# Kernel optimization log

Hardware: AMD Instinct MI355X
Metric: run time of the kernel (lower is better)

Reference implementation:

```python
import jax, jax.numpy as jnp
import numpy as np

B, T, D, H = 2, 2048, 768, 12
d = D // H
FRAG, K_SEL, G = 16, 6, 4
TOP_U, PROTO = 12, 32
ALPHA, GAMMA = 0.2, 0.2
W_MEAN, W_MAX, W_TOPK, W_STD = 1.0, 0.6, 0.4, 0.2
TOPK_FRAC = 0.2
TAU = 8.0
NEG = -1e9


def _norm(x, eps=1e-6):
    return x / jnp.maximum(jnp.linalg.norm(x, axis=-1, keepdims=True), eps)


def setup_inputs():
    key = jax.random.key(0)
    ks = jax.random.split(key, 5)
    s = 0.02
    return {
        'x': jax.random.normal(ks[0], (B, T, D), jnp.float32),
        'Wq': jax.random.normal(ks[1], (D, D), jnp.float32) * s,
        'bq': jnp.zeros((D,), jnp.float32),
        'Wk': jax.random.normal(ks[2], (D, D), jnp.float32) * s,
        'bk': jnp.zeros((D,), jnp.float32),
        'Wv': jax.random.normal(ks[3], (D, D), jnp.float32) * s,
        'bv': jnp.zeros((D,), jnp.float32),
        'Wo': jax.random.normal(ks[4], (D, D), jnp.float32) * s,
        'bo': jnp.zeros((D,), jnp.float32),
    }


def _forward(x, Wq, bq, Wk, bk, Wv, bv, Wo, bo):
    scaling = d ** -0.5

    def shape(t):  # [B,T,D] -> [B*H,T,d]  (BartAttention._shape layout: (b,h))
        return t.reshape(B, T, H, d).transpose(0, 2, 1, 3).reshape(B * H, T, d)

    q = shape((x @ Wq.T + bq) * scaling)
    k = shape(x @ Wk.T + bk)
    v = shape(x @ Wv.T + bv)

    # ---- windowed local candidate indices (build_indices_encoder) ----
    half = FRAG // 2
    t_ar = jnp.arange(T)
    starts = jnp.clip(t_ar - half, 0, T - FRAG)
    idx = starts[:, None] + jnp.arange(FRAG)[None, :]            # [T,F]
    prior = jnp.exp(-jnp.abs(idx - t_ar[:, None]).astype(jnp.float32) / TAU)

    keys_win = k[:, idx]                                          # [BH,T,F,d]
    scores_win = jnp.einsum('btd,btfd->btf', q, keys_win)
    blended = scores_win + ALPHA * prior[None]

    # ---- greedy diversity-penalized top-k (WindowSelector.select_greedy) ----
    kvn = _norm(keys_win)
    f_ar = jnp.arange(FRAG)
    tmp = blended
    sels = []
    for r in range(K_SEL):
        j = jnp.argmax(tmp, -1)                                   # [BH,T]
        sels.append(j)
        if r < K_SEL - 1:
            sel_vec = jnp.take_along_axis(kvn, j[:, :, None, None], axis=2)[:, :, 0]
            cos = jnp.maximum(jnp.sum(kvn * sel_vec[:, :, None, :], -1), 0.0)
            tmp = tmp - GAMMA * cos
        tmp = jnp.where(f_ar[None, None, :] == j[..., None], NEG, tmp)
    sel_local = jnp.stack(sels, -1)                               # [BH,T,k]
    sel_abs = jnp.take_along_axis(
        jnp.broadcast_to(idx[None], (B * H, T, FRAG)), sel_local, axis=-1)

    # ---- per-head global tokens (GlobalChooser.choose_packed) ----
    # faithful to torch: key_states.view(H, bsz, Tk, d).mean(dim=1)
    Kmean = k.reshape(H, B, T, d).mean(1)
    Kbar = _norm(Kmean)
    q_summary = _norm(q.reshape(H, B, T, d).mean(1))
    idxp = jnp.round(jnp.linspace(0.0, T - 1, PROTO)).astype(jnp.int32)
    Qp = q_summary[:, idxp]                                       # [H,P,d]
    S = jax.nn.relu(jnp.einsum('hkd,hpd->hkp', Kbar, Qp))         # [H,T,P]
    kq = max(1, int(round(PROTO * TOPK_FRAC)))
    u = (W_MEAN * S.mean(-1) + W_MAX * S.max(-1)
         + W_TOPK * jax.lax.top_k(S, kq)[0].mean(-1)
         + W_STD * jnp.std(S, axis=-1, ddof=1))
    U = min(TOP_U, T)
    u_vals, top_idx = jax.lax.top_k(u, U)                         # [H,U]
    S_sub = jnp.take_along_axis(S, top_idx[:, :, None], axis=1)   # [H,U,P]
    hr = jnp.arange(H)
    m = jnp.zeros((H, PROTO), S.dtype)
    blocked = jnp.zeros((H, U), bool)
    chosen = []
    for r in range(G):  # greedy facility-location
        gains = jnp.maximum(S_sub - m[:, None, :], 0.0).sum(-1)
        gains = jnp.where(blocked, NEG, gains)
        j = jnp.argmax(gains, 1)
        chosen.append(j)
        blocked = blocked.at[hr, j].set(True)
        m = jnp.maximum(m, S_sub[hr, j])
    chosen_abs = jnp.take_along_axis(top_idx, jnp.stack(chosen, 1), axis=1)  # [H,G]

    # ---- sparse attention over local + global candidates ----
    glob = jnp.broadcast_to(chosen_abs[None], (B, H, G)).reshape(B * H, G)
    cand = jnp.concatenate(
        [sel_abs, jnp.broadcast_to(glob[:, None, :], (B * H, T, G))], -1)  # [BH,T,k+g]
    Ksel = jax.vmap(lambda kk, ii: kk[ii])(k, cand)               # [BH,T,k+g,d]
    Vsel = jax.vmap(lambda vv, ii: vv[ii])(v, cand)
    attn = jax.nn.softmax(jnp.einsum('btd,btcd->btc', q, Ksel), axis=-1)
    out = jnp.einsum('btc,btcd->btd', attn, Vsel)
    out = out.reshape(B, H, T, d).transpose(0, 2, 1, 3).reshape(B, T, D)
    return out @ Wo.T + bo


def reference(x, Wq, bq, Wk, bk, Wv, bv, Wo, bo):
    return _forward(x, Wq, bq, Wk, bk, Wv, bv, Wo, bo)
```

## Files before the change

### kernel.cpp

```cpp
#include <hip/hip_runtime.h>
#include <math.h>

#define TSEQ 2048
#define DM   768
#define NH   12
#define HD   64
#define NBH  24
#define WN   589824

typedef __attribute__((ext_vector_type(8))) short short8;
typedef __attribute__((ext_vector_type(8))) _Float16 half8;
typedef __attribute__((ext_vector_type(4))) float f32x4;

#define MFMA_F16(a, b, c)  __builtin_amdgcn_mfma_f32_16x16x32_f16(a, b, c, 0, 0, 0)

__constant__ int c_idxp[32] = {0,66,132,198,264,330,396,462,528,594,660,726,
  792,858,924,990,1057,1123,1189,1255,1321,1387,1453,1519,1585,1651,1717,1783,
  1849,1915,1981,2047};

template <int CTRL>
__device__ __forceinline__ float dppf(float x) {
  return __int_as_float(__builtin_amdgcn_mov_dpp(__float_as_int(x), CTRL, 0xF, 0xF, true));
}
template <int CTRL>
__device__ __forceinline__ int dppi(int x) {
  return __builtin_amdgcn_mov_dpp(x, CTRL, 0xF, 0xF, true);
}
__device__ __forceinline__ float wsum(float v) {
  v += dppf<0x121>(v);
  v += dppf<0x122>(v);
  v += dppf<0x124>(v);
  v += dppf<0x128>(v);
  v += __shfl_xor(v, 16, 64);
  v += __shfl_xor(v, 32, 64);
  return v;
}
__device__ __forceinline__ float wmaxr(float v) {
  v = fmaxf(v, dppf<0x121>(v));
  v = fmaxf(v, dppf<0x122>(v));
  v = fmaxf(v, dppf<0x124>(v));
  v = fmaxf(v, dppf<0x128>(v));
  v = fmaxf(v, __shfl_xor(v, 16, 64));
  v = fmaxf(v, __shfl_xor(v, 32, 64));
  return v;
}
__device__ __forceinline__ float rowsum16(float v) {
  v += dppf<0x121>(v); v += dppf<0x122>(v);
  v += dppf<0x124>(v); v += dppf<0x128>(v);
  return v;
}
__device__ __forceinline__ float rowmax16(float v) {
  v = fmaxf(v, dppf<0x121>(v)); v = fmaxf(v, dppf<0x122>(v));
  v = fmaxf(v, dppf<0x124>(v)); v = fmaxf(v, dppf<0x128>(v));
  return v;
}
__device__ __forceinline__ int rowmin16i(int v) {
  v = min(v, dppi<0x121>(v)); v = min(v, dppi<0x122>(v));
  v = min(v, dppi<0x124>(v)); v = min(v, dppi<0x128>(v));
  return v;
}

__device__ __forceinline__ void split16(const float4& v0, const float4& v1,
                                        ushort* ph, ushort* pl) {
  float xs[8] = {v0.x, v0.y, v0.z, v0.w, v1.x, v1.y, v1.z, v1.w};
  half8 h, l;
#pragma unroll
  for (int j = 0; j < 8; ++j) {
    _Float16 hb = (_Float16)xs[j];
    h[j] = hb;
    float d = xs[j] - (float)hb;
    l[j] = (_Float16)d;
  }
  *(half8*)ph = h;
  *(half8*)pl = l;
}

__device__ __forceinline__ int lds_idx(int row, int chunk ) {
  int line = row >> 1;
  int c8 = ((row & 1) << 2) | chunk;
  return line * 64 + ((c8 ^ (line & 7)) << 3);
}
__device__ __forceinline__ int qoff(int p, int c8) {
  return p * 64 + (((c8 ^ (p & 7)) & 7) << 3);
}

__global__ __launch_bounds__(256) void convert_kernel(
    const float* __restrict__ x,
    const float* __restrict__ W0, const float* __restrict__ W1,
    const float* __restrict__ W2, const float* __restrict__ W3,
    ushort* __restrict__ Xh, ushort* __restrict__ Xl,
    ushort* __restrict__ wsp) {
  int z = blockIdx.y;
  size_t base = (size_t)(blockIdx.x * 256 + threadIdx.x) * 8;
  if (z == 0) {
    float4 v0 = *(const float4*)(x + base);
    float4 v1 = *(const float4*)(x + base + 4);
    split16(v0, v1, Xh + base, Xl + base);
  } else {
    if (base >= WN) return;
    int mi = z - 1;
    const float* s = (mi == 0) ? W0 : (mi == 1) ? W1 : (mi == 2) ? W2 : W3;
    ushort* h = wsp + (size_t)mi * 2 * WN;
    float4 v0 = *(const float4*)(s + base);
    float4 v1 = *(const float4*)(s + base + 4);
    split16(v0, v1, h + base, h + WN + base);
  }
}

template <int MODE, int NPROD>
__device__ __forceinline__ void gemm_mfma_body(
    const ushort* __restrict__ Agh, const ushort* __restrict__ Agl,
    const ushort* __restrict__ Bgh, const ushort* __restrict__ Bgl,
    const float* __restrict__ bias, float* __restrict__ dst, float scale,
    int mblk, int nblk, ushort* lds) {
  const int tid = threadIdx.x;
  const int lane = tid & 63;
  const int w = tid >> 6;
  const int wr = w >> 1, wc = w & 1;
  const int lrow = lane & 15, kq = lane >> 4;
  constexpr int ABUF = 4096;
  constexpr int BBUF = 2048;
  ushort* Ahs = lds;
  ushort* Als = Ahs + ABUF;
  ushort* Bhs = lds + 2 * ABUF;
  ushort* Bls = Bhs + BBUF;

  const int arow = tid >> 2;
  const int achk = tid & 3;
  const int aoff0 = lds_idx(arow, achk);
  const int aoff1 = lds_idx(arow + 64, achk);
  const int boff = lds_idx(arow, achk);

  const size_t a0 = (size_t)(mblk + arow) * DM + achk * 8;
  const size_t a1 = (size_t)(mblk + 64 + arow) * DM + achk * 8;
  const size_t b0 = (size_t)(nblk + arow) * DM + achk * 8;

  f32x4 acc[4][2];
#pragma unroll
  for (int i = 0; i < 4; ++i)
#pragma unroll
    for (int j = 0; j < 2; ++j) {
      f32x4 z = {0.f, 0.f, 0.f, 0.f};
      acc[i][j] = z;
    }

  short8 pah0 = *(const short8*)(Agh + a0), pah1 = *(const short8*)(Agh + a1);
  short8 pal0 = *(const short8*)(Agl + a0), pal1 = *(const short8*)(Agl + a1);
  short8 pbh = *(const short8*)(Bgh + b0);
  short8 pbl = *(const short8*)(Bgl + b0);

  for (int k0 = 0; k0 < DM; k0 += 32) {
    __syncthreads();
    *(short8*)&Ahs[aoff0] = pah0; *(short8*)&Ahs[aoff1] = pah1;
    *(short8*)&Als[aoff0] = pal0; *(short8*)&Als[aoff1] = pal1;
    *(short8*)&Bhs[boff] = pbh;
    *(short8*)&Bls[boff] = pbl;
    __syncthreads();
    if (k0 + 32 < DM) {
      pah0 = *(const short8*)(Agh + a0 + k0 + 32);
      pah1 = *(const short8*)(Agh + a1 + k0 + 32);
      pal0 = *(const short8*)(Agl + a0 + k0 + 32);
      pal1 = *(const short8*)(Agl + a1 + k0 + 32);
      pbh = *(const short8*)(Bgh + b0 + k0 + 32);
      pbl = *(const short8*)(Bgl + b0 + k0 + 32);
    }
    half8 afh[4], afl[4];
#pragma unroll
    for (int fi = 0; fi < 4; ++fi) {
      int o = lds_idx(wr * 64 + fi * 16 + lrow, kq);
      afh[fi] = *(const half8*)&Ahs[o];
      afl[fi] = *(const half8*)&Als[o];
    }
#pragma unroll
    for (int fj = 0; fj < 2; ++fj) {
      int o = lds_idx(wc * 32 + fj * 16 + lrow, kq);
      half8 bfh = *(const half8*)&Bhs[o];
      half8 bfl = *(const half8*)&Bls[o];
#pragma unroll
      for (int fi = 0; fi < 4; ++fi) {
        acc[fi][fj] = MFMA_F16(afh[fi], bfh, acc[fi][fj]);
        acc[fi][fj] = MFMA_F16(afl[fi], bfh, acc[fi][fj]);
        acc[fi][fj] = MFMA_F16(afh[fi], bfl, acc[fi][fj]);
        if (NPROD == 4) {
          acc[fi][fj] = MFMA_F16(afl[fi], bfl, acc[fi][fj]);
        }
      }
    }
  }

#pragma unroll
  for (int fj = 0; fj < 2; ++fj) {
    int col = nblk + wc * 32 + fj * 16 + lrow;
    float bv = bias[col];
#pragma unroll
    for (int fi = 0; fi < 4; ++fi) {
#pragma unroll
      for (int reg = 0; reg < 4; ++reg) {
        int row = mblk + wr * 64 + fi * 16 + kq * 4 + reg;
        float o = (acc[fi][fj][reg] + bv) * scale;
        if (MODE == 0) {
          dst[(size_t)row * DM + col] = o;
        } else {
          int b_ = row >> 11, t = row & (TSEQ - 1);
          int h = col >> 6, dd = col & 63;
          dst[(((size_t)(b_ * NH + h)) * TSEQ + t) * HD + dd] = o;
        }
      }
    }
  }
}

__global__ __launch_bounds__(256) void qkv_kernel(
    const ushort* __restrict__ Xh, const ushort* __restrict__ Xl,
    const ushort* __restrict__ wsp,
    const float* __restrict__ bq, float* __restrict__ qd,
    const float* __restrict__ bk, float* __restrict__ kd,
    const float* __restrict__ bv, float* __restrict__ vd) {
  __shared__ ushort lds[2 * 4096 + 2 * 2048];
  int lid = blockIdx.x + 12 * blockIdx.y + 384 * blockIdx.z;
  int swz = (lid & 7) * 144 + (lid >> 3);
  int z = swz / 384;
  int rem = swz - z * 384;
  int wy = rem / 12, wx = rem - wy * 12;
  const ushort* Bb = wsp + (size_t)z * 2 * WN;
  if (z == 2) {
    gemm_mfma_body<1, 3>(Xh, Xl, Bb, Bb + WN,
                         bv, vd, 1.0f, wy * 128, wx * 64, lds);
  } else {
    gemm_mfma_body<1, 4>(Xh, Xl, Bb, Bb + WN,
                         z ? bk : bq, z ? kd : qd, z ? 1.0f : 0.125f,
                         wy * 128, wx * 64, lds);
  }
}

__global__ __launch_bounds__(256) void oproj_kernel(
    const ushort* __restrict__ Ph, const ushort* __restrict__ Pl,
    const ushort* __restrict__ wsp,
    const float* __restrict__ bias, float* __restrict__ dst) {
  __shared__ ushort lds[2 * 4096 + 2 * 2048];
  int lid = blockIdx.x + 12 * blockIdx.y;
  int swz = (lid & 7) * 48 + (lid >> 3);
  int wy = swz / 12, wx = swz - wy * 12;
  const ushort* Bb = wsp + (size_t)3 * 2 * WN;
  gemm_mfma_body<0, 3>(Ph, Pl, Bb, Bb + WN,
                       bias, dst, 1.0f, wy * 128, wx * 64, lds);
}

__global__ __launch_bounds__(256) void window_kernel(
    const float* __restrict__ q, const float* __restrict__ k,
    int* __restrict__ sel) {
  int wid = blockIdx.x * 4 + (threadIdx.x >> 6);
  int lane = threadIdx.x & 63;
  int f = lane & 15, kq = lane >> 4;
  int bh = wid >> 11, t = wid & (TSEQ - 1);
  int start = t - 8;
  if (start < 0) start = 0;
  if (start > TSEQ - 16) start = TSEQ - 16;

  const float* kp = k + ((size_t)bh * TSEQ + start + f) * HD + kq * 8;
  const float* qp = q + ((size_t)bh * TSEQ + t) * HD + kq * 8;
  float kv[16], qv[16];
  *(float4*)&kv[0]  = *(const float4*)(kp + 0);
  *(float4*)&kv[4]  = *(const float4*)(kp + 4);
  *(float4*)&kv[8]  = *(const float4*)(kp + 32);
  *(float4*)&kv[12] = *(const float4*)(kp + 36);
  *(float4*)&qv[0]  = *(const float4*)(qp + 0);
  *(float4*)&qv[4]  = *(const float4*)(qp + 4);
  *(float4*)&qv[8]  = *(const float4*)(qp + 32);
  *(float4*)&qv[12] = *(const float4*)(qp + 36);

  float sp = 0.f, np = 0.f;
#pragma unroll
  for (int i = 0; i < 16; ++i) { sp = fmaf(qv[i], kv[i], sp); np = fmaf(kv[i], kv[i], np); }
  sp += __shfl_xor(sp, 16, 64); sp += __shfl_xor(sp, 32, 64);
  np += __shfl_xor(np, 16, 64); np += __shfl_xor(np, 32, 64);
  float nrm = fmaxf(sqrtf(np), 1e-6f);
  float kn[16];
#pragma unroll
  for (int i = 0; i < 16; ++i) kn[i] = kv[i] / nrm;

  half8 h0, l0, h1, l1;
#pragma unroll
  for (int j = 0; j < 8; ++j) {
    _Float16 hb = (_Float16)kn[j];
    h0[j] = hb;
    l0[j] = (_Float16)(kn[j] - (float)hb);
    _Float16 hb1 = (_Float16)kn[8 + j];
    h1[j] = hb1;
    l1[j] = (_Float16)(kn[8 + j] - (float)hb1);
  }
  f32x4 g = {0.f, 0.f, 0.f, 0.f};
  g = MFMA_F16(h0, h0, g); g = MFMA_F16(h1, h1, g);
  g = MFMA_F16(l0, h0, g); g = MFMA_F16(l1, h1, g);
  g = MFMA_F16(h0, l0, g); g = MFMA_F16(h1, l1, g);
  g = MFMA_F16(l0, l0, g); g = MFMA_F16(l1, l1, g);

  int dist = start + f - t; if (dist < 0) dist = -dist;
  float tmp = sp + 0.2f * expf(-(float)dist * 0.125f);

  int* selp = sel + ((size_t)bh * TSEQ + t) * 6;
#pragma unroll
  for (int r = 0; r < 6; ++r) {
    float best = tmp; int bj = f;
    {
      float ov = dppf<0x121>(best); int oi = dppi<0x121>(bj);
      if (ov > best || (ov == best && oi < bj)) { best = ov; bj = oi; }
      ov = dppf<0x122>(best); oi = dppi<0x122>(bj);
      if (ov > best || (ov == best && oi < bj)) { best = ov; bj = oi; }
      ov = dppf<0x124>(best); oi = dppi<0x124>(bj);
      if (ov > best || (ov == best && oi < bj)) { best = ov; bj = oi; }
      ov = dppf<0x128>(best); oi = dppi<0x128>(bj);
      if (ov > best || (ov == best && oi < bj)) { best = ov; bj = oi; }
    }
    if (lane == 0) selp[r] = start + bj;
    if (r < 5) {
      float s01 = (bj & 1) ? g[1] : g[0];
      float s23 = (bj & 1) ? g[3] : g[2];
      float gsel = (bj & 2) ? s23 : s01;
      float grow = __shfl(gsel, ((bj >> 2) << 4) | f, 64);
      tmp -= 0.2f * fmaxf(grow, 0.f);
    }
    if (f == bj) tmp = -1e9f;
  }
}

__global__ __launch_bounds__(256) void qp_kernel(const float* __restrict__ q,
                                                 ushort* __restrict__ Qph,
                                                 ushort* __restrict__ Qpl) {
  int wid = blockIdx.x * 4 + (threadIdx.x >> 6);
  int lane = threadIdx.x & 63;
  int a = wid >> 5, p = wid & 31;
  int t = c_idxp[p];
  float v = 0.5f * (q[((size_t)(2 * a) * TSEQ + t) * HD + lane] +
                    q[((size_t)(2 * a + 1) * TSEQ + t) * HD + lane]);
  float n2 = wsum(v * v);
  float nrm = fmaxf(sqrtf(n2), 1e-6f);
  float qn = v / nrm;
  _Float16 hb = (_Float16)qn;
  float d = qn - (float)hb;
  size_t idx = ((size_t)a * 32 + p) * HD + lane;
  Qph[idx] = __builtin_bit_cast(ushort, hb);
  _Float16 lb = (_Float16)d;
  Qpl[idx] = __builtin_bit_cast(ushort, lb);
}

__global__ __launch_bounds__(256) void proto_score_kernel(
    const float* __restrict__ k,
    const ushort* __restrict__ Qph, const ushort* __restrict__ Qpl,
    float* __restrict__ S, float* __restrict__ u) {
  int a = blockIdx.y;
  __shared__ ushort Qh[2048], Ql[2048];
  {
    int p = threadIdx.x >> 3, c8 = threadIdx.x & 7;
    size_t src = (size_t)a * 2048 + p * 64 + c8 * 8;
    *(short8*)&Qh[qoff(p, c8)] = *(const short8*)(Qph + src);
    *(short8*)&Ql[qoff(p, c8)] = *(const short8*)(Qpl + src);
  }
  __syncthreads();

  int wv = threadIdx.x >> 6, lane = threadIdx.x & 63;
  int f = lane & 15, kq = lane >> 4;
  int tbase = blockIdx.x * 64 + wv * 16;
  int tl = tbase + f;

  const float* k0p = k + ((size_t)(2 * a) * TSEQ + tl) * HD + kq * 8;
  const float* k1p = k + ((size_t)(2 * a + 1) * TSEQ + tl) * HD + kq * 8;
  float km[16];
  {
    float4 x0 = *(const float4*)(k0p + 0),  y0 = *(const float4*)(k1p + 0);
    float4 x1 = *(const float4*)(k0p + 4),  y1 = *(const float4*)(k1p + 4);
    float4 x2 = *(const float4*)(k0p + 32), y2 = *(const float4*)(k1p + 32);
    float4 x3 = *(const float4*)(k0p + 36), y3 = *(const float4*)(k1p + 36);
    km[0] = 0.5f*(x0.x+y0.x); km[1] = 0.5f*(x0.y+y0.y);
    km[2] = 0.5f*(x0.z+y0.z); km[3] = 0.5f*(x0.w+y0.w);
    km[4] = 0.5f*(x1.x+y1.x); km[5] = 0.5f*(x1.y+y1.y);
    km[6] = 0.5f*(x1.z+y1.z); km[7] = 0.5f*(x1.w+y1.w);
    km[8] = 0.5f*(x2.x+y2.x); km[9] = 0.5f*(x2.y+y2.y);
    km[10] = 0.5f*(x2.z+y2.z); km[11] = 0.5f*(x2.w+y2.w);
    km[12] = 0.5f*(x3.x+y3.x); km[13] = 0.5f*(x3.y+y3.y);
    km[14] = 0.5f*(x3.z+y3.z); km[15] = 0.5f*(x3.w+y3.w);
  }
  float np = 0.f;
#pragma unroll
  for (int i = 0; i < 16; ++i) np = fmaf(km[i], km[i], np);
  np += __shfl_xor(np, 16, 64); np += __shfl_xor(np, 32, 64);
  float nrm = fmaxf(sqrtf(np), 1e-6f);

  half8 ah[2], al[2];
#pragma unroll
  for (int s = 0; s < 2; ++s)
#pragma unroll
    for (int j = 0; j < 8; ++j) {
      float x = km[s * 8 + j] / nrm;
      _Float16 hb = (_Float16)x;
      ah[s][j] = hb;
      al[s][j] = (_Float16)(x - (float)hb);
    }

  f32x4 acc0 = {0.f, 0.f, 0.f, 0.f}, acc1 = {0.f, 0.f, 0.f, 0.f};
#pragma unroll
  for (int s = 0; s < 2; ++s) {
    half8 b0h = *(const half8*)&Qh[qoff(f, s * 4 + kq)];
    half8 b0l = *(const half8*)&Ql[qoff(f, s * 4 + kq)];
    half8 b1h = *(const half8*)&Qh[qoff(16 + f, s * 4 + kq)];
    half8 b1l = *(const half8*)&Ql[qoff(16 + f, s * 4 + kq)];
    acc0 = MFMA_F16(ah[s], b0h, acc0);
    acc0 = MFMA_F16(al[s], b0h, acc0);
    acc0 = MFMA_F16(ah[s], b0l, acc0);
    acc0 = MFMA_F16(al[s], b0l, acc0);
    acc1 = MFMA_F16(ah[s], b1h, acc1);
    acc1 = MFMA_F16(al[s], b1h, acc1);
    acc1 = MFMA_F16(ah[s], b1l, acc1);
    acc1 = MFMA_F16(al[s], b1l, acc1);
  }

#pragma unroll
  for (int reg = 0; reg < 4; ++reg) {
    float s0 = fmaxf(acc0[reg], 0.f);
    float s1 = fmaxf(acc1[reg], 0.f);
    int t = tbase + kq * 4 + reg;
    size_t srow = ((size_t)a * TSEQ + t) * 32;
    S[srow + f] = s0;
    S[srow + 16 + f] = s1;
    float mean = rowsum16(s0 + s1) / 32.0f;
    float mx = rowmax16(fmaxf(s0, s1));
    float cur0 = s0, cur1 = s1;
    float topsum = 0.f;
#pragma unroll
    for (int r = 0; r < 6; ++r) {
      float mm = rowmax16(fmaxf(cur0, cur1));
      topsum += mm;
      int i0 = rowmin16i((cur0 == mm) ? f : 999);
      int i1 = rowmin16i((cur1 == mm) ? f : 999);
      bool take0 = (i0 < 999);
      if (take0 && f == i0) cur0 = -1e30f;
      if (!take0 && f == i1) cur1 = -1e30f;
    }
    float d0 = s0 - mean, d1 = s1 - mean;
    float sd = sqrtf(rowsum16(d0 * d0 + d1 * d1) / 31.0f);
    float uval = ((1.0f * mean + 0.6f * mx) + 0.4f * (topsum / 6.0f)) + 0.2f * sd;
    if (f == 0) u[(size_t)a * TSEQ + t] = uval;
  }
}

__global__ void head_select_kernel(const float* __restrict__ u,
                                   const float* __restrict__ S,
                                   int* __restrict__ glob) {
  int a = blockIdx.x;
  int lane = threadIdx.x;
  float uv[32];
#pragma unroll
  for (int c = 0; c < 32; ++c) uv[c] = u[(size_t)a * TSEQ + c * 64 + lane];
  unsigned removed = 0;
  int tidx = 0;
#pragma unroll
  for (int r = 0; r < 12; ++r) {
    float best = -1e30f; int bidx = 1 << 30;
#pragma unroll
    for (int c = 0; c < 32; ++c) {
      if (!((removed >> c) & 1u)) {
        float vv = uv[c]; int gi = c * 64 + lane;
        if (vv > best || (vv == best && gi < bidx)) { best = vv; bidx = gi; }
      }
    }
#pragma unroll
    for (int mS = 1; mS < 64; mS <<= 1) {
      float ov = __shfl_xor(best, mS, 64);
      int oi = __shfl_xor(bidx, mS, 64);
      if (ov > best || (ov == best && oi < bidx)) { best = ov; bidx = oi; }
    }
    if (lane == (bidx & 63)) removed |= 1u << (bidx >> 6);
    if (lane == r) tidx = bidx;
  }
  float srow[12];
#pragma unroll
  for (int r = 0; r < 12; ++r) {
    int tr = __shfl(tidx, r, 64);
    srow[r] = (lane < 32) ? S[((size_t)a * TSEQ + tr) * 32 + lane] : 0.f;
  }
  float m = 0.f;
  unsigned blocked = 0;
#pragma unroll
  for (int g = 0; g < 4; ++g) {
    float gains[12];
#pragma unroll
    for (int r = 0; r < 12; ++r) {
      float gr = (lane < 32) ? fmaxf(srow[r] - m, 0.f) : 0.f;
      gains[r] = wsum(gr);
    }
    float best = -1e30f; int bj = 0;
#pragma unroll
    for (int r = 0; r < 12; ++r) {
      float vv = ((blocked >> r) & 1u) ? -1e9f : gains[r];
      if (vv > best) { best = vv; bj = r; }
    }
    blocked |= 1u << bj;
#pragma unroll
    for (int r = 0; r < 12; ++r) m = (r == bj) ? fmaxf(m, srow[r]) : m;
    int gidx = __shfl(tidx, bj, 64);
    if (lane == 0) glob[a * 4 + g] = gidx;
  }
}

__global__ __launch_bounds__(256) void attend_kernel(
    const float* __restrict__ q, const float* __restrict__ k,
    const float* __restrict__ v, const int* __restrict__ sel,
    const int* __restrict__ glob, ushort* __restrict__ Ph,
    ushort* __restrict__ Pl) {
  int wid = blockIdx.x * 4 + (threadIdx.x >> 6);
  int lane = threadIdx.x & 63;
  int bh = wid >> 11, t = wid & (TSEQ - 1);
  int h = bh % NH, b = bh / NH;
  float qv = q[((size_t)bh * TSEQ + t) * HD + lane];
  int cand[10];
  const int* selp = sel + ((size_t)bh * TSEQ + t) * 6;
#pragma unroll
  for (int c = 0; c < 6; ++c) cand[c] = selp[c];
#pragma unroll
  for (int c = 0; c < 4; ++c) cand[6 + c] = glob[h * 4 + c];
  float sc[10];
#pragma unroll
  for (int c = 0; c < 10; ++c) {
    float kv = k[((size_t)bh * TSEQ + cand[c]) * HD + lane];
    sc[c] = wsum(qv * kv);
  }
  float mx = sc[0];
#pragma unroll
  for (int c = 1; c < 10; ++c) mx = fmaxf(mx, sc[c]);
  float e[10], den = 0.f;
#pragma unroll
  for (int c = 0; c < 10; ++c) { e[c] = expf(sc[c] - mx); den += e[c]; }
  float o = 0.f;
#pragma unroll
  for (int c = 0; c < 10; ++c) {
    float w = e[c] / den;
    o += w * v[((size_t)bh * TSEQ + cand[c]) * HD + lane];
  }
  size_t idx = ((size_t)b * TSEQ + t) * DM + h * HD + lane;
  _Float16 hb = (_Float16)o;
  float d = o - (float)hb;
  Ph[idx] = __builtin_bit_cast(ushort, hb);
  _Float16 lb = (_Float16)d;
  Pl[idx] = __builtin_bit_cast(ushort, lb);
}

extern "C" void kernel_launch(void* const* d_in, const int* in_sizes, int n_in,
                              void* d_out, int out_size, void* d_ws, size_t ws_size,
                              hipStream_t stream) {
  const float* x  = (const float*)d_in[0];
  const float* Wq = (const float*)d_in[1];
  const float* bq = (const float*)d_in[2];
  const float* Wk = (const float*)d_in[3];
  const float* bk = (const float*)d_in[4];
  const float* Wv = (const float*)d_in[5];
  const float* bv = (const float*)d_in[6];
  const float* Wo = (const float*)d_in[7];
  const float* bo = (const float*)d_in[8];
  float* out = (float*)d_out;

  float* ws = (float*)d_ws;
  const size_t QKV = (size_t)NBH * TSEQ * HD;
  float* qb = ws;
  float* kb = qb + QKV;
  float* vb = kb + QKV;
  float* slotA = vb + QKV;
  float* QpSlot = slotA + QKV;
  float* S  = QpSlot + (size_t)NH * 32 * HD;
  float* u  = S + (size_t)NH * TSEQ * 32;
  int* sel  = (int*)(u + (size_t)NH * TSEQ);
  int* glob = sel + (size_t)NBH * TSEQ * 6;
  ushort* wsp = (ushort*)(glob + 64);

  ushort* Xh = (ushort*)slotA;
  ushort* Xl = Xh + QKV;
  ushort* Ph = Xh;
  ushort* Pl = Xl;
  ushort* Qph = (ushort*)QpSlot;
  ushort* Qpl = Qph + (size_t)NH * 32 * HD;

  convert_kernel<<<dim3(1536, 5), 256, 0, stream>>>(
      x, Wq, Wk, Wv, Wo, Xh, Xl, wsp);
  qkv_kernel<<<dim3(12, 32, 3), 256, 0, stream>>>(
      Xh, Xl, wsp, bq, qb, bk, kb, bv, vb);
  window_kernel<<<12288, 256, 0, stream>>>(qb, kb, sel);
  qp_kernel<<<96, 256, 0, stream>>>(qb, Qph, Qpl);
  proto_score_kernel<<<dim3(32, NH), 256, 0, stream>>>(kb, Qph, Qpl, S, u);
  head_select_kernel<<<NH, 64, 0, stream>>>(u, S, glob);
  attend_kernel<<<12288, 256, 0, stream>>>(qb, kb, vb, sel, glob, Ph, Pl);
  oproj_kernel<<<dim3(12, 32), 256, 0, stream>>>(Ph, Pl, wsp, bo, out);
}
```

Measured before the change: 217.1 us.

## Fuse window, prototype and head-select kernels into one launch with last-block election

Merges the window-selection, prototype-query normalisation, prototype scoring and head-select kernels into a single select_kernel. Block ranges are dispatched by blockIdx. Each prototype-scoring block recomputes the normalised prototype queries into LDS itself, and the last block per head (found with an atomic counter) runs the greedy head selection. The weight conversion grid is compacted so no blocks go idle. This removes three kernel launches and their gaps, at the cost of a memset, threadfence/atomic traffic, and redundant prototype-query computation in every scoring block.

```diff
diff --git a/kernel.cpp b/kernel.cpp
--- a/kernel.cpp
+++ b/kernel.cpp
@@ -35,15 +35,6 @@
   v += __shfl_xor(v, 32, 64);
   return v;
 }
-__device__ __forceinline__ float wmaxr(float v) {
-  v = fmaxf(v, dppf<0x121>(v));
-  v = fmaxf(v, dppf<0x122>(v));
-  v = fmaxf(v, dppf<0x124>(v));
-  v = fmaxf(v, dppf<0x128>(v));
-  v = fmaxf(v, __shfl_xor(v, 16, 64));
-  v = fmaxf(v, __shfl_xor(v, 32, 64));
-  return v;
-}
 __device__ __forceinline__ float rowsum16(float v) {
   v += dppf<0x121>(v); v += dppf<0x122>(v);
   v += dppf<0x124>(v); v += dppf<0x128>(v);
@@ -90,15 +81,16 @@
     const float* __restrict__ W2, const float* __restrict__ W3,
     ushort* __restrict__ Xh, ushort* __restrict__ Xl,
     ushort* __restrict__ wsp) {
-  int z = blockIdx.y;
-  size_t base = (size_t)(blockIdx.x * 256 + threadIdx.x) * 8;
-  if (z == 0) {
+  int bid = blockIdx.x;
+  if (bid < 1536) {
+    size_t base = ((size_t)bid * 256 + threadIdx.x) * 8;
     float4 v0 = *(const float4*)(x + base);
     float4 v1 = *(const float4*)(x + base + 4);
     split16(v0, v1, Xh + base, Xl + base);
   } else {
-    if (base >= WN) return;
-    int mi = z - 1;
+    int r = bid - 1536;
+    int mi = r / 288, sub = r - mi * 288;
+    size_t base = ((size_t)sub * 256 + threadIdx.x) * 8;
     const float* s = (mi == 0) ? W0 : (mi == 1) ? W1 : (mi == 2) ? W2 : W3;
     ushort* h = wsp + (size_t)mi * 2 * WN;
     float4 v0 = *(const float4*)(s + base);
@@ -246,121 +238,127 @@
                        bias, dst, 1.0f, wy * 128, wx * 64, lds);
 }
 
-__global__ __launch_bounds__(256) void window_kernel(
+__global__ __launch_bounds__(256) void select_kernel(
     const float* __restrict__ q, const float* __restrict__ k,
-    int* __restrict__ sel) {
-  int wid = blockIdx.x * 4 + (threadIdx.x >> 6);
-  int lane = threadIdx.x & 63;
+    int* __restrict__ sel, float* __restrict__ S, float* __restrict__ u,
+    int* __restrict__ glob, int* __restrict__ cnt) {
+  __shared__ ushort Qh[2048], Ql[2048];
+  int wv = threadIdx.x >> 6, lane = threadIdx.x & 63;
+
+  if (blockIdx.x < 12288) {
+    int wid = blockIdx.x * 4 + wv;
+    int f = lane & 15, kq = lane >> 4;
+    int bh = wid >> 11, t = wid & (TSEQ - 1);
+    int start = t - 8;
+    if (start < 0) start = 0;
+    if (start > TSEQ - 16) start = TSEQ - 16;
+
+    const float* kp = k + ((size_t)bh * TSEQ + start + f) * HD + kq * 8;
+    const float* qp = q + ((size_t)bh * TSEQ + t) * HD + kq * 8;
+    float kv[16], qv[16];
+    *(float4*)&kv[0]  = *(const float4*)(kp + 0);
+    *(float4*)&kv[4]  = *(const float4*)(kp + 4);
+    *(float4*)&kv[8]  = *(const float4*)(kp + 32);
+    *(float4*)&kv[12] = *(const float4*)(kp + 36);
+    *(float4*)&qv[0]  = *(const float4*)(qp + 0);
+    *(float4*)&qv[4]  = *(const float4*)(qp + 4);
+    *(float4*)&qv[8]  = *(const float4*)(qp + 32);
+    *(float4*)&qv[12] = *(const float4*)(qp + 36);
+
+    float sp = 0.f, np = 0.f;
+#pragma unroll
+    for (int i = 0; i < 16; ++i) { sp = fmaf(qv[i], kv[i], sp); np = fmaf(kv[i], kv[i], np); }
+    sp += __shfl_xor(sp, 16, 64); sp += __shfl_xor(sp, 32, 64);
+    np += __shfl_xor(np, 16, 64); np += __shfl_xor(np, 32, 64);
+    float nrm = fmaxf(sqrtf(np), 1e-6f);
+    float kn[16];
+#pragma unroll
+    for (int i = 0; i < 16; ++i) kn[i] = kv[i] / nrm;
+
+    half8 h0, l0, h1, l1;
+#pragma unroll
+    for (int j = 0; j < 8; ++j) {
+      _Float16 hb = (_Float16)kn[j];
+      h0[j] = hb;
+      l0[j] = (_Float16)(kn[j] - (float)hb);
+      _Float16 hb1 = (_Float16)kn[8 + j];
+      h1[j] = hb1;
+      l1[j] = (_Float16)(kn[8 + j] - (float)hb1);
+    }
+    f32x4 g = {0.f, 0.f, 0.f, 0.f};
+    g = MFMA_F16(h0, h0, g); g = MFMA_F16(h1, h1, g);
+    g = MFMA_F16(l0, h0, g); g = MFMA_F16(l1, h1, g);
+    g = MFMA_F16(h0, l0, g); g = MFMA_F16(h1, l1, g);
+    g = MFMA_F16(l0, l0, g); g = MFMA_F16(l1, l1, g);
+
+    int dist = start + f - t; if (dist < 0) dist = -dist;
+    float tmp = sp + 0.2f * expf(-(float)dist * 0.125f);
+
+    int* selp = sel + ((size_t)bh * TSEQ + t) * 6;
+#pragma unroll
+    for (int r = 0; r < 6; ++r) {
+      float best = tmp; int bj = f;
+      {
+        float ov = dppf<0x121>(best); int oi = dppi<0x121>(bj);
+        if (ov > best || (ov == best && oi < bj)) { best = ov; bj = oi; }
+        ov = dppf<0x122>(best); oi = dppi<0x122>(bj);
+        if (ov > best || (ov == best && oi < bj)) { best = ov; bj = oi; }
+        ov = dppf<0x124>(best); oi = dppi<0x124>(bj);
+        if (ov > best || (ov == best && oi < bj)) { best = ov; bj = oi; }
+        ov = dppf<0x128>(best); oi = dppi<0x128>(bj);
+        if (ov > best || (ov == best && oi < bj)) { best = ov; bj = oi; }
+      }
+      if (lane == 0) selp[r] = start + bj;
+      if (r < 5) {
+        float s01 = (bj & 1) ? g[1] : g[0];
+        float s23 = (bj & 1) ? g[3] : g[2];
+        float gsel = (bj & 2) ? s23 : s01;
+        float grow = __shfl(gsel, ((bj >> 2) << 4) | f, 64);
+        tmp -= 0.2f * fmaxf(grow, 0.f);
+      }
+      if (f == bj) tmp = -1e9f;
+    }
+    return;
+  }
+
+  int bid2 = blockIdx.x - 12288;
+  int a = bid2 >> 5;
+  int tb = bid2 & 31;
+
+  {
+    int p = wv * 8 + (lane >> 3);
+    int c8 = lane & 7;
+    int t = c_idxp[p];
+    const float* q0 = q + ((size_t)(2 * a) * TSEQ + t) * HD + c8 * 8;
+    const float* q1 = q + ((size_t)(2 * a + 1) * TSEQ + t) * HD + c8 * 8;
+    float4 x0 = *(const float4*)q0, x1 = *(const float4*)(q0 + 4);
+    float4 y0 = *(const float4*)q1, y1 = *(const float4*)(q1 + 4);
+    float vv[8] = {0.5f * (x0.x + y0.x), 0.5f * (x0.y + y0.y),
+                   0.5f * (x0.z + y0.z), 0.5f * (x0.w + y0.w),
+                   0.5f * (x1.x + y1.x), 0.5f * (x1.y + y1.y),
+                   0.5f * (x1.z + y1.z), 0.5f * (x1.w + y1.w)};
+    float ssq = 0.f;
+#pragma unroll
+    for (int j = 0; j < 8; ++j) ssq = fmaf(vv[j], vv[j], ssq);
+    ssq += __shfl_xor(ssq, 1, 64);
+    ssq += __shfl_xor(ssq, 2, 64);
+    ssq += __shfl_xor(ssq, 4, 64);
+    float nrm = fmaxf(sqrtf(ssq), 1e-6f);
+    half8 qh, ql_;
+#pragma unroll
+    for (int j = 0; j < 8; ++j) {
+      float xx = vv[j] / nrm;
+      _Float16 hb = (_Float16)xx;
+      qh[j] = hb;
+      ql_[j] = (_Float16)(xx - (float)hb);
+    }
+    *(half8*)&Qh[qoff(p, c8)] = qh;
+    *(half8*)&Ql[qoff(p, c8)] = ql_;
+  }
+  __syncthreads();
+
   int f = lane & 15, kq = lane >> 4;
-  int bh = wid >> 11, t = wid & (TSEQ - 1);
-  int start = t - 8;
-  if (start < 0) start = 0;
-  if (start > TSEQ - 16) start = TSEQ - 16;
-
-  const float* kp = k + ((size_t)bh * TSEQ + start + f) * HD + kq * 8;
-  const float* qp = q + ((size_t)bh * TSEQ + t) * HD + kq * 8;
-  float kv[16], qv[16];
-  *(float4*)&kv[0]  = *(const float4*)(kp + 0);
-  *(float4*)&kv[4]  = *(const float4*)(kp + 4);
-  *(float4*)&kv[8]  = *(const float4*)(kp + 32);
-  *(float4*)&kv[12] = *(const float4*)(kp + 36);
-  *(float4*)&qv[0]  = *(const float4*)(qp + 0);
-  *(float4*)&qv[4]  = *(const float4*)(qp + 4);
-  *(float4*)&qv[8]  = *(const float4*)(qp + 32);
-  *(float4*)&qv[12] = *(const float4*)(qp + 36);
-
-  float sp = 0.f, np = 0.f;
-#pragma unroll
-  for (int i = 0; i < 16; ++i) { sp = fmaf(qv[i], kv[i], sp); np = fmaf(kv[i], kv[i], np); }
-  sp += __shfl_xor(sp, 16, 64); sp += __shfl_xor(sp, 32, 64);
-  np += __shfl_xor(np, 16, 64); np += __shfl_xor(np, 32, 64);
-  float nrm = fmaxf(sqrtf(np), 1e-6f);
-  float kn[16];
-#pragma unroll
-  for (int i = 0; i < 16; ++i) kn[i] = kv[i] / nrm;
-
-  half8 h0, l0, h1, l1;
-#pragma unroll
-  for (int j = 0; j < 8; ++j) {
-    _Float16 hb = (_Float16)kn[j];
-    h0[j] = hb;
-    l0[j] = (_Float16)(kn[j] - (float)hb);
-    _Float16 hb1 = (_Float16)kn[8 + j];
-    h1[j] = hb1;
-    l1[j] = (_Float16)(kn[8 + j] - (float)hb1);
-  }
-  f32x4 g = {0.f, 0.f, 0.f, 0.f};
-  g = MFMA_F16(h0, h0, g); g = MFMA_F16(h1, h1, g);
-  g = MFMA_F16(l0, h0, g); g = MFMA_F16(l1, h1, g);
-  g = MFMA_F16(h0, l0, g); g = MFMA_F16(h1, l1, g);
-  g = MFMA_F16(l0, l0, g); g = MFMA_F16(l1, l1, g);
-
-  int dist = start + f - t; if (dist < 0) dist = -dist;
-  float tmp = sp + 0.2f * expf(-(float)dist * 0.125f);
-
-  int* selp = sel + ((size_t)bh * TSEQ + t) * 6;
-#pragma unroll
-  for (int r = 0; r < 6; ++r) {
-    float best = tmp; int bj = f;
-    {
-      float ov = dppf<0x121>(best); int oi = dppi<0x121>(bj);
-      if (ov > best || (ov == best && oi < bj)) { best = ov; bj = oi; }
-      ov = dppf<0x122>(best); oi = dppi<0x122>(bj);
-      if (ov > best || (ov == best && oi < bj)) { best = ov; bj = oi; }
-      ov = dppf<0x124>(best); oi = dppi<0x124>(bj);
-      if (ov > best || (ov == best && oi < bj)) { best = ov; bj = oi; }
-      ov = dppf<0x128>(best); oi = dppi<0x128>(bj);
-      if (ov > best || (ov == best && oi < bj)) { best = ov; bj = oi; }
-    }
-    if (lane == 0) selp[r] = start + bj;
-    if (r < 5) {
-      float s01 = (bj & 1) ? g[1] : g[0];
-      float s23 = (bj & 1) ? g[3] : g[2];
-      float gsel = (bj & 2) ? s23 : s01;
-      float grow = __shfl(gsel, ((bj >> 2) << 4) | f, 64);
-      tmp -= 0.2f * fmaxf(grow, 0.f);
-    }
-    if (f == bj) tmp = -1e9f;
-  }
-}
-
-__global__ __launch_bounds__(256) void qp_kernel(const float* __restrict__ q,
-                                                 ushort* __restrict__ Qph,
-                                                 ushort* __restrict__ Qpl) {
-  int wid = blockIdx.x * 4 + (threadIdx.x >> 6);
-  int lane = threadIdx.x & 63;
-  int a = wid >> 5, p = wid & 31;
-  int t = c_idxp[p];
-  float v = 0.5f * (q[((size_t)(2 * a) * TSEQ + t) * HD + lane] +
-                    q[((size_t)(2 * a + 1) * TSEQ + t) * HD + lane]);
-  float n2 = wsum(v * v);
-  float nrm = fmaxf(sqrtf(n2), 1e-6f);
-  float qn = v / nrm;
-  _Float16 hb = (_Float16)qn;
-  float d = qn - (float)hb;
-  size_t idx = ((size_t)a * 32 + p) * HD + lane;
-  Qph[idx] = __builtin_bit_cast(ushort, hb);
-  _Float16 lb = (_Float16)d;
-  Qpl[idx] = __builtin_bit_cast(ushort, lb);
-}
-
-__global__ __launch_bounds__(256) void proto_score_kernel(
-    const float* __restrict__ k,
-    const ushort* __restrict__ Qph, const ushort* __restrict__ Qpl,
-    float* __restrict__ S, float* __restrict__ u) {
-  int a = blockIdx.y;
-  __shared__ ushort Qh[2048], Ql[2048];
-  {
-    int p = threadIdx.x >> 3, c8 = threadIdx.x & 7;
-    size_t src = (size_t)a * 2048 + p * 64 + c8 * 8;
-    *(short8*)&Qh[qoff(p, c8)] = *(const short8*)(Qph + src);
-    *(short8*)&Ql[qoff(p, c8)] = *(const short8*)(Qpl + src);
-  }
-  __syncthreads();
-
-  int wv = threadIdx.x >> 6, lane = threadIdx.x & 63;
-  int f = lane & 15, kq = lane >> 4;
-  int tbase = blockIdx.x * 64 + wv * 16;
+  int tbase = tb * 64 + wv * 16;
   int tl = tbase + f;
 
   const float* k0p = k + ((size_t)(2 * a) * TSEQ + tl) * HD + kq * 8;
@@ -441,64 +439,68 @@
     float uval = ((1.0f * mean + 0.6f * mx) + 0.4f * (topsum / 6.0f)) + 0.2f * sd;
     if (f == 0) u[(size_t)a * TSEQ + t] = uval;
   }
-}
-
-__global__ void head_select_kernel(const float* __restrict__ u,
-                                   const float* __restrict__ S,
-                                   int* __restrict__ glob) {
-  int a = blockIdx.x;
-  int lane = threadIdx.x;
-  float uv[32];
-#pragma unroll
-  for (int c = 0; c < 32; ++c) uv[c] = u[(size_t)a * TSEQ + c * 64 + lane];
-  unsigned removed = 0;
-  int tidx = 0;
-#pragma unroll
-  for (int r = 0; r < 12; ++r) {
-    float best = -1e30f; int bidx = 1 << 30;
-#pragma unroll
-    for (int c = 0; c < 32; ++c) {
-      if (!((removed >> c) & 1u)) {
-        float vv = uv[c]; int gi = c * 64 + lane;
-        if (vv > best || (vv == best && gi < bidx)) { best = vv; bidx = gi; }
-      }
-    }
-#pragma unroll
-    for (int mS = 1; mS < 64; mS <<= 1) {
-      float ov = __shfl_xor(best, mS, 64);
-      int oi = __shfl_xor(bidx, mS, 64);
-      if (ov > best || (ov == best && oi < bidx)) { best = ov; bidx = oi; }
-    }
-    if (lane == (bidx & 63)) removed |= 1u << (bidx >> 6);
-    if (lane == r) tidx = bidx;
-  }
-  float srow[12];
-#pragma unroll
-  for (int r = 0; r < 12; ++r) {
-    int tr = __shfl(tidx, r, 64);
-    srow[r] = (lane < 32) ? S[((size_t)a * TSEQ + tr) * 32 + lane] : 0.f;
-  }
-  float m = 0.f;
-  unsigned blocked = 0;
-#pragma unroll
-  for (int g = 0; g < 4; ++g) {
-    float gains[12];
-#pragma unroll
-    for (int r = 0; r < 12; ++r) {
-      float gr = (lane < 32) ? fmaxf(srow[r] - m, 0.f) : 0.f;
-      gains[r] = wsum(gr);
-    }
-    float best = -1e30f; int bj = 0;
-#pragma unroll
-    for (int r = 0; r < 12; ++r) {
-      float vv = ((blocked >> r) & 1u) ? -1e9f : gains[r];
-      if (vv > best) { best = vv; bj = r; }
-    }
-    blocked |= 1u << bj;
-#pragma unroll
-    for (int r = 0; r < 12; ++r) m = (r == bj) ? fmaxf(m, srow[r]) : m;
-    int gidx = __shfl(tidx, bj, 64);
-    if (lane == 0) glob[a * 4 + g] = gidx;
+
+  __threadfence();
+  __syncthreads();
+  if (threadIdx.x < 64) {
+    int old = 0;
+    if (lane == 0) old = atomicAdd(&cnt[a], 1);
+    old = __shfl(old, 0, 64);
+    if (old == 31) {
+      __threadfence();
+      float uv[32];
+#pragma unroll
+      for (int c = 0; c < 32; ++c) uv[c] = u[(size_t)a * TSEQ + c * 64 + lane];
+      unsigned removed = 0;
+      int tidx = 0;
+#pragma unroll
+      for (int r = 0; r < 12; ++r) {
+        float best = -1e30f; int bidx = 1 << 30;
+#pragma unroll
+        for (int c = 0; c < 32; ++c) {
+          if (!((removed >> c) & 1u)) {
+            float vv = uv[c]; int gi = c * 64 + lane;
+            if (vv > best || (vv == best && gi < bidx)) { best = vv; bidx = gi; }
+          }
+        }
+#pragma unroll
+        for (int mS = 1; mS < 64; mS <<= 1) {
+          float ov = __shfl_xor(best, mS, 64);
+          int oi = __shfl_xor(bidx, mS, 64);
+          if (ov > best || (ov == best && oi < bidx)) { best = ov; bidx = oi; }
+        }
+        if (lane == (bidx & 63)) removed |= 1u << (bidx >> 6);
+        if (lane == r) tidx = bidx;
+      }
+      float srow[12];
+#pragma unroll
+      for (int r = 0; r < 12; ++r) {
+        int tr = __shfl(tidx, r, 64);
+        srow[r] = (lane < 32) ? S[((size_t)a * TSEQ + tr) * 32 + lane] : 0.f;
+      }
+      float m = 0.f;
+      unsigned blocked = 0;
+#pragma unroll
+      for (int g = 0; g < 4; ++g) {
+        float gains[12];
+#pragma unroll
+        for (int r = 0; r < 12; ++r) {
+          float gr = (lane < 32) ? fmaxf(srow[r] - m, 0.f) : 0.f;
+          gains[r] = wsum(gr);
+        }
+        float best = -1e30f; int bj = 0;
+#pragma unroll
+        for (int r = 0; r < 12; ++r) {
+          float vv = ((blocked >> r) & 1u) ? -1e9f : gains[r];
+          if (vv > best) { best = vv; bj = r; }
+        }
+        blocked |= 1u << bj;
+#pragma unroll
+        for (int r = 0; r < 12; ++r) m = (r == bj) ? fmaxf(m, srow[r]) : m;
+        int gidx = __shfl(tidx, bj, 64);
+        if (lane == 0) glob[a * 4 + g] = gidx;
+      }
+    }
   }
 }
 
@@ -569,23 +571,19 @@
   float* u  = S + (size_t)NH * TSEQ * 32;
   int* sel  = (int*)(u + (size_t)NH * TSEQ);
   int* glob = sel + (size_t)NBH * TSEQ * 6;
+  int* cnt  = glob + 48;
   ushort* wsp = (ushort*)(glob + 64);
 
   ushort* Xh = (ushort*)slotA;
   ushort* Xl = Xh + QKV;
   ushort* Ph = Xh;
   ushort* Pl = Xl;
-  ushort* Qph = (ushort*)QpSlot;
-  ushort* Qpl = Qph + (size_t)NH * 32 * HD;
-
-  convert_kernel<<<dim3(1536, 5), 256, 0, stream>>>(
-      x, Wq, Wk, Wv, Wo, Xh, Xl, wsp);
+
+  hipMemsetAsync(cnt, 0, 12 * sizeof(int), stream);
+  convert_kernel<<<2688, 256, 0, stream>>>(x, Wq, Wk, Wv, Wo, Xh, Xl, wsp);
   qkv_kernel<<<dim3(12, 32, 3), 256, 0, stream>>>(
       Xh, Xl, wsp, bq, qb, bk, kb, bv, vb);
-  window_kernel<<<12288, 256, 0, stream>>>(qb, kb, sel);
-  qp_kernel<<<96, 256, 0, stream>>>(qb, Qph, Qpl);
-  proto_score_kernel<<<dim3(32, NH), 256, 0, stream>>>(kb, Qph, Qpl, S, u);
-  head_select_kernel<<<NH, 64, 0, stream>>>(u, S, glob);
+  select_kernel<<<12672, 256, 0, stream>>>(qb, kb, sel, S, u, glob, cnt);
   attend_kernel<<<12288, 256, 0, stream>>>(qb, kb, vb, sel, glob, Ph, Pl);
   oproj_kernel<<<dim3(12, 32), 256, 0, stream>>>(Ph, Pl, wsp, bo, out);
 }
```

Result: slower. 251.2 us (+15.7%).
